# Kernel tuning notes

Hardware: AMD Instinct MI355X
Metric: run time of the kernel (lower is better)

## Reference

```python
import jax, jax.numpy as jnp
import numpy as np

PH, PW = 7, 7  # pooled_height, pooled_width
B, H, W, C, R = 4, 64, 64, 256, 128


def setup_inputs() -> dict:
    key = jax.random.key(0)
    k1, k2, k3 = jax.random.split(key, 3)
    feature_map = jax.random.normal(k1, (B, H, W, C), dtype=jnp.float32)
    # ROIs: (y_min, x_min, y_max, x_max) relative coords; sized so every
    # region has >= PH rows / PW cols (avoids empty-bin -inf edge case).
    start = jax.random.uniform(k2, (B, R, 2), minval=0.0, maxval=0.4)
    extent = jax.random.uniform(k3, (B, R, 2), minval=0.3, maxval=0.55)
    rois = jnp.concatenate([start, start + extent], axis=-1).astype(jnp.float32)
    return {"feature_map": feature_map, "rois": rois}


def _pool_image(fm, rois_img):
    # fm: (H, W, C); rois_img: (R, 4)
    h, w, _ = fm.shape
    # tf.cast(float->int32) truncates; coords are non-negative so == floor
    h0 = jnp.floor(h * rois_img[:, 0]).astype(jnp.int32)
    w0 = jnp.floor(w * rois_img[:, 1]).astype(jnp.int32)
    h1 = jnp.floor(h * rois_img[:, 2]).astype(jnp.int32)
    w1 = jnp.floor(w * rois_img[:, 3]).astype(jnp.int32)
    rh, rw = h1 - h0, w1 - w0
    hstep = jnp.maximum(rh // PH, 1)  # guard: assumes region >= pooled grid
    wstep = jnp.maximum(rw // PW, 1)

    # Map each absolute row/col to its pooled bin (or PH/PW = "outside").
    rel_h = jnp.arange(h)[None, :] - h0[:, None]            # (R, H)
    bin_h = jnp.clip(rel_h // hstep[:, None], 0, PH - 1)     # last bin extends to region end
    row_id = jnp.where((rel_h >= 0) & (rel_h < rh[:, None]), bin_h, PH)
    rel_w = jnp.arange(w)[None, :] - w0[:, None]            # (R, W)
    bin_w = jnp.clip(rel_w // wstep[:, None], 0, PW - 1)
    col_id = jnp.where((rel_w >= 0) & (rel_w < rw[:, None]), bin_w, PW)

    # Stage 1: segment-max over rows -> (R, PH, W, C)
    seg_rows = jax.vmap(
        lambda ids: jax.ops.segment_max(fm, ids, num_segments=PH + 1)
    )(row_id)[:, :PH]

    # Stage 2: segment-max over cols -> (R, PH, PW, C)
    def col_pool(t, ids):  # t: (PH, W, C)
        tt = jnp.swapaxes(t, 0, 1)  # (W, PH, C)
        s = jax.ops.segment_max(tt, ids, num_segments=PW + 1)[:PW]
        return jnp.swapaxes(s, 0, 1)  # (PH, PW, C)

    return jax.vmap(col_pool)(seg_rows, col_id)


def reference(feature_map, rois):
    # (B, R, PH, PW, C)
    return jax.vmap(_pool_image)(feature_map, rois)
```

## Files before the change

### kernel.cpp

```cpp
#include <hip/hip_runtime.h>
#include <math.h>

#define PH 7
#define PW 7
#define BB 4
#define HH 64
#define WW 64
#define CC 256
#define RR 128
#define CH4 (CC / 4)
#define BINS_PER_IMG (RR * PH * PW)
#define NBINS (BB * BINS_PER_IMG)
#define WPB 2
#define NBLK (NBINS / WPB)
#define BLK_PER_SLOT (NBLK / 8)

typedef float f4 __attribute__((ext_vector_type(4)));

__device__ __forceinline__ f4 max4(f4 a, f4 b) {
    f4 r;
    r.x = fmaxf(a.x, b.x); r.y = fmaxf(a.y, b.y);
    r.z = fmaxf(a.z, b.z); r.w = fmaxf(a.w, b.w);
    return r;
}

__global__ __launch_bounds__(128) void ROIPoolingLayer_62079457296467_kernel(
    const float* __restrict__ fm, const float* __restrict__ rois,
    float* __restrict__ out)
{
    const int wave = threadIdx.x >> 6;
    const int lane = threadIdx.x & 63;

    const int bid   = blockIdx.x;
    const int xcd   = bid & 7;
    const int slot  = bid >> 3;
    const int b     = xcd >> 1;
    const int blkin = (xcd & 1) * BLK_PER_SLOT + slot;
    const int local = blkin * WPB + wave;
    const int r     = local / (PH * PW);
    const int bin   = local - r * (PH * PW);
    const int ph    = bin / PW;
    const int pw    = bin - ph * PW;
    const int br    = b * RR + r;

    const f4 roi = ((const f4*)rois)[br];
    const int h0 = (int)floorf((float)HH * roi.x);
    const int w0 = (int)floorf((float)WW * roi.y);
    const int h1 = (int)floorf((float)HH * roi.z);
    const int w1 = (int)floorf((float)WW * roi.w);
    const int rh = h1 - h0;
    const int rw = w1 - w0;
    const int hstep = max(rh / PH, 1);
    const int wstep = max(rw / PW, 1);

    int hs = h0 + ph * hstep;
    int he = (ph == PH - 1) ? (h0 + rh) : (hs + hstep);
    he = min(he, h0 + rh);  he = min(he, HH);
    int ws = w0 + pw * wstep;
    int we = (pw == PW - 1) ? (w0 + rw) : (ws + wstep);
    we = min(we, w0 + rw);  we = min(we, WW);

    const int hbin = he - hs;
    const int wbin = we - ws;
    const int npix = hbin * wbin;

    const f4* __restrict__ bp =
        (const f4*)fm + ((size_t)b * HH + hs) * (WW * CH4) + (size_t)ws * CH4;

    f4 acc = (f4){-INFINITY, -INFINITY, -INFINITY, -INFINITY};

    if (npix > 0) {
        const unsigned m = (65536u + (unsigned)wbin - 1) / (unsigned)wbin;
        f4 bufA[8], bufB[8];

#define LOADR(buf, p0)                                                  \
        _Pragma("unroll")                                               \
        for (int k = 0; k < 8; ++k) {                                   \
            const int pk = min((p0) + k, npix - 1);                     \
            const int q  = (int)(((unsigned)pk * m) >> 16);             \
            const int w  = pk - q * wbin;                               \
            buf[k] = bp[(q * WW + w) * CH4 + lane];                     \
        }
#define CONS(buf)                                                       \
        {                                                               \
            f4 m0 = max4(buf[0], buf[1]);                               \
            f4 m1 = max4(buf[2], buf[3]);                               \
            f4 m2 = max4(buf[4], buf[5]);                               \
            f4 m3 = max4(buf[6], buf[7]);                               \
            acc = max4(acc, max4(max4(m0, m1), max4(m2, m3)));          \
        }

        const int rounds = (npix + 7) >> 3;
        LOADR(bufA, 0)
        int t = 1;
        for (; t + 1 < rounds; t += 2) {
            LOADR(bufB, t * 8)
            CONS(bufA)
            LOADR(bufA, (t + 1) * 8)
            CONS(bufB)
        }
        if (t < rounds) {
            LOADR(bufB, t * 8)
            CONS(bufA)
            CONS(bufB)
        } else {
            CONS(bufA)
        }
#undef LOADR
#undef CONS
    }

    const size_t gbin = (size_t)b * BINS_PER_IMG + local;
    __builtin_nontemporal_store(acc, (f4*)out + gbin * CH4 + lane);
}

extern "C" void kernel_launch(void* const* d_in, const int* in_sizes, int n_in,
                              void* d_out, int out_size, void* d_ws, size_t ws_size,
                              hipStream_t stream) {
    const float* fm   = (const float*)d_in[0];
    const float* rois = (const float*)d_in[1];
    float* out        = (float*)d_out;
    ROIPoolingLayer_62079457296467_kernel<<<NBLK, 128, 0, stream>>>(fm, rois, out);
}
```

Measured before the change: 90.39 us.

## Assign one wave per pooled row and loop over all column bins

Each wave now handles a whole pooled row (roi, ph) and loops over all 7 column bins, instead of one wave per (roi, ph, pw) bin. ROI decode, bin bounds and the magic-divisor constants are computed once per row rather than once per bin, and blocks grow to 4 waves. The cost is 7x fewer waves in flight and serialized per-bin latency inside each wave, which can reduce memory-level parallelism for this load-bound gather.

```diff
diff --git a/kernel.cpp b/kernel.cpp
--- a/kernel.cpp
+++ b/kernel.cpp
@@ -10,9 +10,9 @@
 #define RR 128
 #define CH4 (CC / 4)
 #define BINS_PER_IMG (RR * PH * PW)
-#define NBINS (BB * BINS_PER_IMG)
-#define WPB 2
-#define NBLK (NBINS / WPB)
+#define NROWBINS (BB * RR * PH)
+#define WPB 4
+#define NBLK (NROWBINS / WPB)
 #define BLK_PER_SLOT (NBLK / 8)
 
 typedef float f4 __attribute__((ext_vector_type(4)));
@@ -24,7 +24,7 @@
     return r;
 }
 
-__global__ __launch_bounds__(128) void ROIPoolingLayer_62079457296467_kernel(
+__global__ __launch_bounds__(256) void ROIPoolingLayer_62079457296467_kernel(
     const float* __restrict__ fm, const float* __restrict__ rois,
     float* __restrict__ out)
 {
@@ -37,10 +37,8 @@
     const int b     = xcd >> 1;
     const int blkin = (xcd & 1) * BLK_PER_SLOT + slot;
     const int local = blkin * WPB + wave;
-    const int r     = local / (PH * PW);
-    const int bin   = local - r * (PH * PW);
-    const int ph    = bin / PW;
-    const int pw    = bin - ph * PW;
+    const int r     = local / PH;
+    const int ph    = local - r * PH;
     const int br    = b * RR + r;
 
     const f4 roi = ((const f4*)rois)[br];
@@ -56,62 +54,68 @@
     int hs = h0 + ph * hstep;
     int he = (ph == PH - 1) ? (h0 + rh) : (hs + hstep);
     he = min(he, h0 + rh);  he = min(he, HH);
-    int ws = w0 + pw * wstep;
-    int we = (pw == PW - 1) ? (w0 + rw) : (ws + wstep);
-    we = min(we, w0 + rw);  we = min(we, WW);
+    const int hbin = he - hs;
 
-    const int hbin = he - hs;
-    const int wbin = we - ws;
-    const int npix = hbin * wbin;
+    int wbin6 = rw - (PW - 1) * wstep;
+    wbin6 = min(wbin6, WW - (w0 + (PW - 1) * wstep));
+    const unsigned m_int = (65536u + (unsigned)wstep - 1) / (unsigned)wstep;
+    const unsigned m_6   = (65536u + (unsigned)wbin6 - 1) / (unsigned)wbin6;
 
-    const f4* __restrict__ bp =
-        (const f4*)fm + ((size_t)b * HH + hs) * (WW * CH4) + (size_t)ws * CH4;
+    const int rowbase = (b * HH + hs) * WW;
 
-    f4 acc = (f4){-INFINITY, -INFINITY, -INFINITY, -INFINITY};
+    for (int pw = 0; pw < PW; ++pw) {
+        const int      ws   = w0 + pw * wstep;
+        const int      wbin = (pw == PW - 1) ? wbin6 : wstep;
+        const unsigned m    = (pw == PW - 1) ? m_6 : m_int;
+        const int      npix = hbin * wbin;
 
-    if (npix > 0) {
-        const unsigned m = (65536u + (unsigned)wbin - 1) / (unsigned)wbin;
-        f4 bufA[8], bufB[8];
+        const f4* __restrict__ bp = (const f4*)fm + (size_t)(rowbase + ws) * CH4;
+
+        f4 acc = (f4){-INFINITY, -INFINITY, -INFINITY, -INFINITY};
+
+        if (npix > 0) {
+            f4 bufA[8], bufB[8];
 
 #define LOADR(buf, p0)                                                  \
-        _Pragma("unroll")                                               \
-        for (int k = 0; k < 8; ++k) {                                   \
-            const int pk = min((p0) + k, npix - 1);                     \
-            const int q  = (int)(((unsigned)pk * m) >> 16);             \
-            const int w  = pk - q * wbin;                               \
-            buf[k] = bp[(q * WW + w) * CH4 + lane];                     \
-        }
+            _Pragma("unroll")                                           \
+            for (int k = 0; k < 8; ++k) {                               \
+                const int pk = min((p0) + k, npix - 1);                 \
+                const int q  = (int)(((unsigned)pk * m) >> 16);         \
+                const int w  = pk - q * wbin;                           \
+                buf[k] = bp[(q * WW + w) * CH4 + lane];                 \
+            }
 #define CONS(buf)                                                       \
-        {                                                               \
-            f4 m0 = max4(buf[0], buf[1]);                               \
-            f4 m1 = max4(buf[2], buf[3]);                               \
-            f4 m2 = max4(buf[4], buf[5]);                               \
-            f4 m3 = max4(buf[6], buf[7]);                               \
-            acc = max4(acc, max4(max4(m0, m1), max4(m2, m3)));          \
+            {                                                           \
+                f4 m0 = max4(buf[0], buf[1]);                           \
+                f4 m1 = max4(buf[2], buf[3]);                           \
+                f4 m2 = max4(buf[4], buf[5]);                           \
+                f4 m3 = max4(buf[6], buf[7]);                           \
+                acc = max4(acc, max4(max4(m0, m1), max4(m2, m3)));      \
+            }
+
+            const int rounds = (npix + 7) >> 3;
+            LOADR(bufA, 0)
+            int t = 1;
+            for (; t + 1 < rounds; t += 2) {
+                LOADR(bufB, t * 8)
+                CONS(bufA)
+                LOADR(bufA, (t + 1) * 8)
+                CONS(bufB)
+            }
+            if (t < rounds) {
+                LOADR(bufB, t * 8)
+                CONS(bufA)
+                CONS(bufB)
+            } else {
+                CONS(bufA)
+            }
+#undef LOADR
+#undef CONS
         }
 
-        const int rounds = (npix + 7) >> 3;
-        LOADR(bufA, 0)
-        int t = 1;
-        for (; t + 1 < rounds; t += 2) {
-            LOADR(bufB, t * 8)
-            CONS(bufA)
-            LOADR(bufA, (t + 1) * 8)
-            CONS(bufB)
-        }
-        if (t < rounds) {
-            LOADR(bufB, t * 8)
-            CONS(bufA)
-            CONS(bufB)
-        } else {
-            CONS(bufA)
-        }
-#undef LOADR
-#undef CONS
+        const size_t gbin = (size_t)(br * PH + ph) * PW + pw;
+        __builtin_nontemporal_store(acc, (f4*)out + gbin * CH4 + lane);
     }
-
-    const size_t gbin = (size_t)b * BINS_PER_IMG + local;
-    __builtin_nontemporal_store(acc, (f4*)out + gbin * CH4 + lane);
 }
 
 extern "C" void kernel_launch(void* const* d_in, const int* in_sizes, int n_in,
@@ -120,5 +124,5 @@
     const float* fm   = (const float*)d_in[0];
     const float* rois = (const float*)d_in[1];
     float* out        = (float*)d_out;
-    ROIPoolingLayer_62079457296467_kernel<<<NBLK, 128, 0, stream>>>(fm, rois, out);
+    ROIPoolingLayer_62079457296467_kernel<<<NBLK, 256, 0, stream>>>(fm, rois, out);
 }
```

After: 103.9 us. +15.0%, slower.
